# Kernel optimization log

Hardware: AMD Instinct MI355X
Metric: run time of the kernel (lower is better)

Reference implementation:

```python
import jax, jax.numpy as jnp
import numpy as np

T_STEPS = 16384  # sequence length T
N_DIM = 256      # input channels n
M_DIM = 512      # hidden/reservoir size m
K_MEM = 511      # memory rows K (addresses are 0..K, row 0 = 'no memory op')
L_OUT = 256      # output dims L


def setup_inputs() -> dict:
    key = jax.random.key(0)
    ks = jax.random.split(key, 10)
    s_ih = 1.0 / np.sqrt(N_DIM)
    s_hh = 1.0 / np.sqrt(M_DIM)
    X = jax.random.normal(ks[0], (T_STEPS, N_DIM), jnp.float32)
    h0 = jnp.zeros((M_DIM,), jnp.float32)  # init_state = zeros(m)
    # torch.nn.GRU parameters (single layer): weight_ih [3m, n], weight_hh [3m, m]
    W_ih = jax.random.normal(ks[1], (3 * M_DIM, N_DIM), jnp.float32) * s_ih
    W_hh = jax.random.normal(ks[2], (3 * M_DIM, M_DIM), jnp.float32) * s_hh
    b_ih = jax.random.normal(ks[3], (3 * M_DIM,), jnp.float32) * s_hh
    b_hh = jax.random.normal(ks[4], (3 * M_DIM,), jnp.float32) * s_hh
    # C_: Linear(m, K+1) -> memory address logits
    C_w = jax.random.normal(ks[5], (K_MEM + 1, M_DIM), jnp.float32) * s_hh
    C_b = jax.random.normal(ks[6], (K_MEM + 1,), jnp.float32) * s_hh
    # V_: Linear(m, L) -> outputs
    V_w = jax.random.normal(ks[7], (L_OUT, M_DIM), jnp.float32) * s_hh
    V_b = jax.random.normal(ks[8], (L_OUT,), jnp.float32) * s_hh
    return {"X": X, "h0": h0, "W_ih": W_ih, "W_hh": W_hh, "b_ih": b_ih,
            "b_hh": b_hh, "C_w": C_w, "C_b": C_b, "V_w": V_w, "V_b": V_b}


def reference(X, h0, W_ih, W_hh, b_ih, b_hh, C_w, C_b, V_w, V_b):
    m = h0.shape[0]
    n_addr = C_b.shape[0]  # K + 1

    def step(carry, x):
        h, M, written = carry
        # GRU cell (torch semantics)
        gi = W_ih @ x + b_ih          # [3m]
        gh = W_hh @ h + b_hh          # [3m]
        i_r, i_z, i_n = jnp.split(gi, 3)
        h_r, h_z, h_n = jnp.split(gh, 3)
        r = jax.nn.sigmoid(i_r + h_r)
        z = jax.nn.sigmoid(i_z + h_z)
        ng = jnp.tanh(i_n + r * h_n)
        h_new = (1.0 - z) * ng + z * h
        # discrete memory addressing via argmax over C_(h)
        logits = C_w @ h_new + C_b    # [K+1]
        q = jnp.argmax(logits)
        mem_q = M[q]                  # gather (read before write)
        has_entry = written[q] & (q > 0)
        # if address already written: read memory, replacing h
        h_out = jnp.where(has_entry, mem_q, h_new)
        # if address new (and > 0): write h into memory
        do_write = (q > 0) & jnp.logical_not(written[q])
        write_val = jnp.where(do_write, h_new, mem_q)  # no-op write otherwise
        M = M.at[q].set(write_val)
        written = written.at[q].set(written[q] | (q > 0))
        return (h_out, M, written), h_out

    M0 = jnp.zeros((n_addr, m), X.dtype)       # q_0 = 0 -> memory starts empty
    written0 = jnp.zeros((n_addr,), jnp.bool_)
    _, H = jax.lax.scan(step, (h0, M0, written0), X)  # H: [T, m]
    Y = H @ V_w.T + V_b                          # [T, L]
    return Y
```

## Files before the change

kernel.cpp:

```cpp
#include <hip/hip_runtime.h>
#include <stdint.h>

#define T_STEPS 16384
#define NDIM 256
#define MDIM 512
#define KP1 512
#define LOUT 256
#define G 16
#define TPB 256

typedef unsigned long long u64;
typedef unsigned int u32;

constexpr size_t OFF_GH    = 0;
constexpr size_t OFF_GHS   = 512ull * 1536;
constexpr size_t OFF_M     = OFF_GHS + 1536;
constexpr size_t OFF_RING  = OFF_M + 512ull * 512;
constexpr size_t OFF_H     = OFF_RING + 4ull * 1536;
constexpr size_t OFF_VWT   = OFF_H + 16384ull * 512;
constexpr size_t OFF_FLAGS = OFF_VWT + 512ull * 256;

__device__ __forceinline__ float ld_cohf(const float* p) {
  return __hip_atomic_load(p, __ATOMIC_RELAXED, __HIP_MEMORY_SCOPE_AGENT);
}
__device__ __forceinline__ void st_cohf(float* p, float v) {
  __hip_atomic_store(p, v, __ATOMIC_RELAXED, __HIP_MEMORY_SCOPE_AGENT);
}
__device__ __forceinline__ u64 ld_flag(const u64* p) {
  return __hip_atomic_load(p, __ATOMIC_RELAXED, __HIP_MEMORY_SCOPE_AGENT);
}
__device__ __forceinline__ void st_flag_rel(u64* p, u64 v) {
  __hip_atomic_store(p, v, __ATOMIC_RELEASE, __HIP_MEMORY_SCOPE_AGENT);
}
__device__ __forceinline__ void st_flag_rlx(u64* p, u64 v) {
  __hip_atomic_store(p, v, __ATOMIC_RELAXED, __HIP_MEMORY_SCOPE_AGENT);
}

__device__ __forceinline__ float sigm(float x) {
  return __builtin_amdgcn_rcpf(1.0f + __expf(-x));
}
__device__ __forceinline__ float tanh_(float x) {
  return 1.0f - 2.0f * __builtin_amdgcn_rcpf(__expf(2.0f * x) + 1.0f);
}

template<int CTRL>
__device__ __forceinline__ u32 dppmax(u32 v) {
  u32 t = (u32)__builtin_amdgcn_update_dpp(0, (int)v, CTRL, 0xf, 0xf, true);
  return v > t ? v : t;
}
__device__ __forceinline__ u32 wave_max_u32(u32 v) {
  v = dppmax<0x111>(v);
  v = dppmax<0x112>(v);
  v = dppmax<0x114>(v);
  v = dppmax<0x118>(v);
  v = dppmax<0x142>(v);
  v = dppmax<0x143>(v);
  return (u32)__builtin_amdgcn_readlane((int)v, 63);
}
__device__ __forceinline__ u32 row16_max_u32(u32 v) {
  v = dppmax<0x111>(v);
  v = dppmax<0x112>(v);
  v = dppmax<0x114>(v);
  v = dppmax<0x118>(v);
  return (u32)__builtin_amdgcn_readlane((int)v, 15);
}

__global__ __launch_bounds__(TPB, 1) void dmm_main(
    const float* __restrict__ X, const float* __restrict__ h0,
    const float* __restrict__ W_ih, const float* __restrict__ W_hh,
    const float* __restrict__ b_ih, const float* __restrict__ b_hh,
    const float* __restrict__ C_w, const float* __restrict__ C_b,
    float* __restrict__ ws)
{
  const int b   = blockIdx.x;
  const int tid = threadIdx.x;
  const int w   = tid >> 6;
  const int l   = tid & 63;

  float* GH   = ws + OFF_GH;
  float* GHS  = ws + OFF_GHS;
  float* Mrow = ws + OFF_M;
  float* RING = ws + OFF_RING;
  float* H    = ws + OFF_H;
  u64*   F    = (u64*)(ws + OFF_FLAGS);

  __shared__ __align__(16) float hnew[MDIM];
  __shared__ __align__(16) float red[96 * 36];
  __shared__ u32 written[KP1];
  __shared__ u32 bcw;

  const int pw   = (w >= 1) ? (w - 1) : 0;
  const int rloc = pw * 32 + (l >> 4) * 8;
  float wih[8][16];
  {
    int rbase = 96 * b + rloc;
    int cbase = 16 * (l & 15);
#pragma unroll
    for (int i = 0; i < 8; i++)
#pragma unroll
      for (int k = 0; k < 16; k++)
        wih[i][k] = W_ih[(size_t)(rbase + i) * NDIM + cbase + k];
  }
  float bihr[8];
#pragma unroll
  for (int i = 0; i < 8; i++) bihr[i] = b_ih[96 * b + rloc + i];

  float cw[4][16];
  {
    int rbase = 32 * b + w * 8 + (l >> 5) * 4;
    int cbase = 16 * (l & 31);
#pragma unroll
    for (int i = 0; i < 4; i++)
#pragma unroll
      for (int k = 0; k < 16; k++)
        cw[i][k] = C_w[(size_t)(rbase + i) * MDIM + cbase + k];
  }

  for (int i = tid; i < KP1; i += TPB) written[i] = 0u;
  if (tid == 0) bcw = 0u;
  hnew[tid]       = h0[tid];
  hnew[tid + 256] = h0[tid + 256];
  __syncthreads();

  float xreg[16];
  auto prefetchX = [&](int s) {
    int cbase = 16 * (l & 15);
#pragma unroll
    for (int k = 0; k < 16; k++) xreg[k] = X[(size_t)s * NDIM + cbase + k];
  };

  auto produce_gi = [&](int s) {
    float p[8];
#pragma unroll
    for (int i = 0; i < 8; i++) {
      float a = 0.f;
#pragma unroll
      for (int k = 0; k < 16; k++) a = fmaf(wih[i][k], xreg[k], a);
      p[i] = a;
    }
#pragma unroll
    for (int off = 1; off <= 8; off <<= 1) {
#pragma unroll
      for (int i = 0; i < 8; i++) p[i] += __shfl_xor(p[i], off, 64);
    }
    if ((l & 15) == 0) {
      float* dst = &RING[(size_t)(s & 3) * 1536 + 96 * b + rloc];
#pragma unroll
      for (int i = 0; i < 8; i++) st_cohf(&dst[i], p[i] + bihr[i]);
    }
  };

  auto compute_gh = [&](float* dst) {
    int cb = 16 * (l & 31);
    float hr[16];
#pragma unroll
    for (int k = 0; k < 16; k += 4) *(float4*)&hr[k] = *(const float4*)&hnew[cb + k];
    int rb = 96 * b + w * 24 + (l >> 5) * 12;
    float p[12];
#pragma unroll
    for (int i = 0; i < 12; i++) {
      float a = 0.f;
      const float* wr = &W_hh[(size_t)(rb + i) * MDIM + cb];
#pragma unroll
      for (int k = 0; k < 16; k++) a = fmaf(wr[k], hr[k], a);
      p[i] = a;
    }
    int rl = w * 24 + (l >> 5) * 12;
    int lc = l & 31;
#pragma unroll
    for (int i = 0; i < 12; i++) red[(rl + i) * 36 + lc] = p[i];
    __syncthreads();
    if (tid < 96) {
      float a = 0.f;
#pragma unroll
      for (int k = 0; k < 32; k += 4) {
        float4 v = *(const float4*)&red[tid * 36 + k];
        a += v.x + v.y + v.z + v.w;
      }
      a += b_hh[96 * b + tid];
      st_cohf(&dst[96 * b + tid], a);
    }
    __syncthreads();
  };

  if (w >= 1) {
    prefetchX(0); produce_gi(0);
    prefetchX(1); produce_gi(1);
    prefetchX(2); produce_gi(2);
    prefetchX(3);
  }
  __syncthreads();
  compute_gh(GHS);
  if (tid == 0) st_flag_rel(&F[b], 1ull);
  if (w == 0) {
    int guard = 0;
    bool done = false;
    while (!done) {
      u64 v = (l < G) ? ld_flag(&F[l]) : 1ull;
      done = (__ballot((int)(v == 1ull)) == ~0ull);
      if (++guard > (1 << 22)) break;
    }
  }
  __syncthreads();

  const float* ghsrc = GHS;
  bool prevReadHit = false;
  int  qprev = 0;

  for (int t = 0; t < T_STEPS; ++t) {
    float g0 = ld_cohf(&ghsrc[tid]);
    float g1 = ld_cohf(&ghsrc[tid + 256]);
    float g2 = ld_cohf(&ghsrc[512 + tid]);
    float g3 = ld_cohf(&ghsrc[512 + tid + 256]);
    float g4 = ld_cohf(&ghsrc[1024 + tid]);
    float g5 = ld_cohf(&ghsrc[1024 + tid + 256]);
    float m0 = 0.f, m1 = 0.f;
    if (prevReadHit) {
      m0 = ld_cohf(&Mrow[(size_t)qprev * 512 + tid]);
      m1 = ld_cohf(&Mrow[(size_t)qprev * 512 + tid + 256]);
    }
    const float* gi = &RING[(size_t)(t & 3) * 1536];
    float i0 = ld_cohf(&gi[tid]);
    float i1 = ld_cohf(&gi[tid + 256]);
    float i2 = ld_cohf(&gi[512 + tid]);
    float i3 = ld_cohf(&gi[512 + tid + 256]);
    float i4 = ld_cohf(&gi[1024 + tid]);
    float i5 = ld_cohf(&gi[1024 + tid + 256]);

    if (prevReadHit) {
      H[(size_t)(t - 1) * 512 + tid]       = m0;
      H[(size_t)(t - 1) * 512 + tid + 256] = m1;
    }

    float hp0 = prevReadHit ? m0 : hnew[tid];
    float hp1 = prevReadHit ? m1 : hnew[tid + 256];
    float r0 = sigm(i0 + g0), r1 = sigm(i1 + g1);
    float z0 = sigm(i2 + g2), z1 = sigm(i3 + g3);
    float n0 = tanh_(fmaf(r0, g4, i4)), n1 = tanh_(fmaf(r1, g5, i5));
    float hn0 = fmaf(z0, hp0 - n0, n0);
    float hn1 = fmaf(z1, hp1 - n1, n1);
    hnew[tid]       = hn0;
    hnew[tid + 256] = hn1;
    __syncthreads();

    {
      int cb = 16 * (l & 31);
      float hr[16];
#pragma unroll
      for (int k = 0; k < 16; k += 4) *(float4*)&hr[k] = *(const float4*)&hnew[cb + k];
      float p0 = 0.f, p1 = 0.f, p2 = 0.f, p3 = 0.f;
#pragma unroll
      for (int k = 0; k < 16; k++) {
        p0 = fmaf(cw[0][k], hr[k], p0);
        p1 = fmaf(cw[1][k], hr[k], p1);
        p2 = fmaf(cw[2][k], hr[k], p2);
        p3 = fmaf(cw[3][k], hr[k], p3);
      }
      int rl = w * 8 + (l >> 5) * 4;
      int lc = l & 31;
      red[(rl + 0) * 36 + lc] = p0;
      red[(rl + 1) * 36 + lc] = p1;
      red[(rl + 2) * 36 + lc] = p2;
      red[(rl + 3) * 36 + lc] = p3;
    }
    __syncthreads();

    u64 ownkey = 0;
    if (w <= 1) {
      u32 ord = 0;
      if (l < 32) {
        const float4* rp = (const float4*)&red[l * 36];
        float4 v0 = rp[0], v1 = rp[1], v2 = rp[2], v3 = rp[3];
        float4 v4 = rp[4], v5 = rp[5], v6 = rp[6], v7 = rp[7];
        double d0 = ((double)v0.x + (double)v0.y) + ((double)v0.z + (double)v0.w);
        double d1 = ((double)v1.x + (double)v1.y) + ((double)v1.z + (double)v1.w);
        double d2 = ((double)v2.x + (double)v2.y) + ((double)v2.z + (double)v2.w);
        double d3 = ((double)v3.x + (double)v3.y) + ((double)v3.z + (double)v3.w);
        double d4 = ((double)v4.x + (double)v4.y) + ((double)v4.z + (double)v4.w);
        double d5 = ((double)v5.x + (double)v5.y) + ((double)v5.z + (double)v5.w);
        double d6 = ((double)v6.x + (double)v6.y) + ((double)v6.z + (double)v6.w);
        double d7 = ((double)v7.x + (double)v7.y) + ((double)v7.z + (double)v7.w);
        double a = (((d0 + d1) + (d2 + d3)) + ((d4 + d5) + (d6 + d7)))
                 + (double)C_b[32 * b + l];
        float af = (float)a;
        u32 bits = __float_as_uint(af);
        ord = (bits & 0x80000000u) ? ~bits : (bits | 0x80000000u);
      }
      u32 maxord = wave_max_u32(ord);
      u64 mask = __ballot((int)(ord == maxord));
      int lane = __builtin_ctzll(mask);
      u64 key41 = ((u64)maxord << 9) | (u64)(511 - (32 * b + lane));
      if (tid == 64)
        st_flag_rlx(&F[16 + (size_t)(t & 1) * 16 + b], ((u64)(t + 1) << 41) | key41);
      ownkey = key41;
    }

    if (w >= 1 && t + 3 < T_STEPS) {
      produce_gi(t + 3);
      if (t + 4 < T_STEPS) prefetchX(t + 4);
    }

    u32 info;
    if (w == 0) {
      const bool need = (l < G) && (l != b);
      const u64* fp = &F[16 + (size_t)(t & 1) * 16 + l];
      u64 vp = need ? ld_flag(fp) : 0;
      int guard = 0;
      u64 v;
      for (;;) {
        u64 vn = need ? ld_flag(fp) : 0;
        bool ok = !need || ((vp >> 41) == (u64)(t + 1));
        if (__ballot((int)ok) == ~0ull) { v = vp; break; }
        vp = vn;
        if (++guard > (1 << 22)) { v = vp; break; }
      }
      u64 key = (l < G) ? ((l == b) ? ownkey : (v & ((1ull << 41) - 1))) : 0;
      u32 o = (u32)(key >> 9);
      u32 maxo = row16_max_u32(o);
      u32 cand = (o == maxo && l < G) ? (u32)(key & 511u) : 0u;
      u32 best = row16_max_u32(cand);
      int q = 511 - (int)best;
      u32 vinfo = 0;
      if (l == 0) {
        u32 wr = written[q];
        u32 fresh = (q > 0 && wr == 0u) ? 1u : 0u;
        u32 rhit  = (q > 0 && wr != 0u) ? 1u : 0u;
        if (fresh) written[q] = 1u;
        vinfo = (u32)q | (fresh << 16) | (rhit << 17);
      }
      vinfo = (u32)__builtin_amdgcn_readfirstlane((int)vinfo);
      info = vinfo;
      if (l == 0)
        __hip_atomic_store(&bcw, (vinfo << 4) | ((u32)(t + 1) & 0xFu),
                           __ATOMIC_RELEASE, __HIP_MEMORY_SCOPE_WORKGROUP);
    } else {
      u32 v;
      int guard = 0;
      for (;;) {
        v = __hip_atomic_load(&bcw, __ATOMIC_ACQUIRE, __HIP_MEMORY_SCOPE_WORKGROUP);
        if ((v & 0xFu) == ((u32)(t + 1) & 0xFu)) break;
        if (++guard > (1 << 25)) break;
      }
      info = v >> 4;
    }
    int  q     = (int)(info & 0xFFFFu);
    bool fresh = (info >> 16) & 1u;
    bool rhit  = (info >> 17) & 1u;

    if (!rhit) {
      H[(size_t)t * 512 + tid]       = hnew[tid];
      H[(size_t)t * 512 + tid + 256] = hnew[tid + 256];
      float* dst;
      if (fresh) {
        if (tid < 32) st_cohf(&Mrow[(size_t)q * 512 + 32 * b + tid], hnew[32 * b + tid]);
        dst = &GH[(size_t)q * 1536];
      } else {
        dst = GHS;
      }
      compute_gh(dst);
      if (tid == 0) st_flag_rel(&F[48 + (size_t)(t & 1) * 16 + b], (u64)(t + 1));
      if (w == 0) {
        int guard = 0;
        for (;;) {
          u64 v = (l < G) ? ld_flag(&F[48 + (size_t)(t & 1) * 16 + l]) : 0;
          bool ok = (l >= G) || (v == (u64)(t + 1));
          if (__ballot((int)ok) == ~0ull) break;
          if (++guard > (1 << 22)) break;
        }
      }
      __syncthreads();
      ghsrc = dst;
      prevReadHit = false;
    } else {
      ghsrc = &GH[(size_t)q * 1536];
      prevReadHit = true;
      qprev = q;
    }
  }

  if (prevReadHit) {
    float a = ld_cohf(&Mrow[(size_t)qprev * 512 + tid]);
    float c = ld_cohf(&Mrow[(size_t)qprev * 512 + tid + 256]);
    H[(size_t)(T_STEPS - 1) * 512 + tid]       = a;
    H[(size_t)(T_STEPS - 1) * 512 + tid + 256] = c;
  }
}

__global__ void vw_transpose(const float* __restrict__ Vw, float* __restrict__ VwT) {
  int idx = blockIdx.x * 256 + threadIdx.x;
  int kk = idx >> 8, ll = idx & 255;
  VwT[idx] = Vw[(size_t)ll * MDIM + kk];
}

__global__ __launch_bounds__(256) void y_gemm(const float* __restrict__ Hm,
                                              const float* __restrict__ VwT,
                                              const float* __restrict__ Vb,
                                              float* __restrict__ Y) {
  int t0 = blockIdx.x * 16;
  int tid = threadIdx.x;
  __shared__ __align__(16) float hs[16 * MDIM];
  for (int i = tid; i < 16 * MDIM; i += 256)
    hs[i] = Hm[(size_t)t0 * MDIM + i];
  __syncthreads();
  float acc[16];
  float vb = Vb[tid];
#pragma unroll
  for (int r = 0; r < 16; r++) acc[r] = vb;
  for (int k = 0; k < MDIM; k += 4) {
    float v0 = VwT[(size_t)(k + 0) * LOUT + tid];
    float v1 = VwT[(size_t)(k + 1) * LOUT + tid];
    float v2 = VwT[(size_t)(k + 2) * LOUT + tid];
    float v3 = VwT[(size_t)(k + 3) * LOUT + tid];
#pragma unroll
    for (int r = 0; r < 16; r++) {
      float4 h4 = *(const float4*)&hs[r * MDIM + k];
      acc[r] = fmaf(h4.x, v0, fmaf(h4.y, v1, fmaf(h4.z, v2, fmaf(h4.w, v3, acc[r]))));
    }
  }
#pragma unroll
  for (int r = 0; r < 16; r++)
    Y[(size_t)(t0 + r) * LOUT + tid] = acc[r];
}

extern "C" void kernel_launch(void* const* d_in, const int* in_sizes, int n_in,
                              void* d_out, int out_size, void* d_ws, size_t ws_size,
                              hipStream_t stream) {
  const float* X    = (const float*)d_in[0];
  const float* h0   = (const float*)d_in[1];
  const float* W_ih = (const float*)d_in[2];
  const float* W_hh = (const float*)d_in[3];
  const float* b_ih = (const float*)d_in[4];
  const float* b_hh = (const float*)d_in[5];
  const float* C_w  = (const float*)d_in[6];
  const float* C_b  = (const float*)d_in[7];
  const float* V_w  = (const float*)d_in[8];
  const float* V_b  = (const float*)d_in[9];
  float* ws  = (float*)d_ws;
  float* VwT = ws + OFF_VWT;
  float* Hm  = ws + OFF_H;

  hipLaunchKernelGGL(vw_transpose, dim3(512), dim3(256), 0, stream, V_w, VwT);
  hipLaunchKernelGGL(dmm_main, dim3(G), dim3(TPB), 0, stream,
                     X, h0, W_ih, W_hh, b_ih, b_hh, C_w, C_b, ws);
  hipLaunchKernelGGL(y_gemm, dim3(T_STEPS / 16), dim3(256), 0, stream,
                     Hm, VwT, V_b, (float*)d_out);
}
```

Before: 43.96 ms.

## Pad inter-block flags to separate lines and compute argmax redundantly per wave

Each 64-bit flag in the global flag array now sits 8 words apart, so the flags no longer share cache lines and polling blocks should contend less. The wave-0 leader that computed the address and handed it to the other waves through a shared-memory mailbox is removed. Every wave now does the row reduction, polls the peer flags and computes the argmax itself, then reads the written table directly. A __syncthreads is added before the written-table update to prevent a race. The cost is more flag polling traffic from all waves and redundant reduction work.

```diff
diff --git a/kernel.cpp b/kernel.cpp
--- a/kernel.cpp
+++ b/kernel.cpp
@@ -87,7 +87,6 @@
   __shared__ __align__(16) float hnew[MDIM];
   __shared__ __align__(16) float red[96 * 36];
   __shared__ u32 written[KP1];
-  __shared__ u32 bcw;
 
   const int pw   = (w >= 1) ? (w - 1) : 0;
   const int rloc = pw * 32 + (l >> 4) * 8;
@@ -117,7 +116,6 @@
   }
 
   for (int i = tid; i < KP1; i += TPB) written[i] = 0u;
-  if (tid == 0) bcw = 0u;
   hnew[tid]       = h0[tid];
   hnew[tid + 256] = h0[tid + 256];
   __syncthreads();
@@ -191,12 +189,12 @@
   }
   __syncthreads();
   compute_gh(GHS);
-  if (tid == 0) st_flag_rel(&F[b], 1ull);
+  if (tid == 0) st_flag_rel(&F[(size_t)b * 8], 1ull);
   if (w == 0) {
     int guard = 0;
     bool done = false;
     while (!done) {
-      u64 v = (l < G) ? ld_flag(&F[l]) : 1ull;
+      u64 v = (l < G) ? ld_flag(&F[(size_t)l * 8]) : 1ull;
       done = (__ballot((int)(v == 1ull)) == ~0ull);
       if (++guard > (1 << 22)) break;
     }
@@ -265,8 +263,8 @@
     }
     __syncthreads();
 
-    u64 ownkey = 0;
-    if (w <= 1) {
+    u64 ownkey;
+    {
       u32 ord = 0;
       if (l < 32) {
         const float4* rp = (const float4*)&red[l * 36];
@@ -289,10 +287,10 @@
       u32 maxord = wave_max_u32(ord);
       u64 mask = __ballot((int)(ord == maxord));
       int lane = __builtin_ctzll(mask);
-      u64 key41 = ((u64)maxord << 9) | (u64)(511 - (32 * b + lane));
+      ownkey = ((u64)maxord << 9) | (u64)(511 - (32 * b + lane));
       if (tid == 64)
-        st_flag_rlx(&F[16 + (size_t)(t & 1) * 16 + b], ((u64)(t + 1) << 41) | key41);
-      ownkey = key41;
+        st_flag_rlx(&F[(16 + (size_t)(t & 1) * 16 + b) * 8],
+                    ((u64)(t + 1) << 41) | ownkey);
     }
 
     if (w >= 1 && t + 3 < T_STEPS) {
@@ -300,10 +298,10 @@
       if (t + 4 < T_STEPS) prefetchX(t + 4);
     }
 
-    u32 info;
-    if (w == 0) {
+    int q;
+    {
       const bool need = (l < G) && (l != b);
-      const u64* fp = &F[16 + (size_t)(t & 1) * 16 + l];
+      const u64* fp = &F[(16 + (size_t)(t & 1) * 16 + l) * 8];
       u64 vp = need ? ld_flag(fp) : 0;
       int guard = 0;
       u64 v;
@@ -319,37 +317,17 @@
       u32 maxo = row16_max_u32(o);
       u32 cand = (o == maxo && l < G) ? (u32)(key & 511u) : 0u;
       u32 best = row16_max_u32(cand);
-      int q = 511 - (int)best;
-      u32 vinfo = 0;
-      if (l == 0) {
-        u32 wr = written[q];
-        u32 fresh = (q > 0 && wr == 0u) ? 1u : 0u;
-        u32 rhit  = (q > 0 && wr != 0u) ? 1u : 0u;
-        if (fresh) written[q] = 1u;
-        vinfo = (u32)q | (fresh << 16) | (rhit << 17);
-      }
-      vinfo = (u32)__builtin_amdgcn_readfirstlane((int)vinfo);
-      info = vinfo;
-      if (l == 0)
-        __hip_atomic_store(&bcw, (vinfo << 4) | ((u32)(t + 1) & 0xFu),
-                           __ATOMIC_RELEASE, __HIP_MEMORY_SCOPE_WORKGROUP);
-    } else {
-      u32 v;
-      int guard = 0;
-      for (;;) {
-        v = __hip_atomic_load(&bcw, __ATOMIC_ACQUIRE, __HIP_MEMORY_SCOPE_WORKGROUP);
-        if ((v & 0xFu) == ((u32)(t + 1) & 0xFu)) break;
-        if (++guard > (1 << 25)) break;
-      }
-      info = v >> 4;
-    }
-    int  q     = (int)(info & 0xFFFFu);
-    bool fresh = (info >> 16) & 1u;
-    bool rhit  = (info >> 17) & 1u;
+      q = 511 - (int)best;
+    }
+    u32 wr = written[q];
+    bool fresh = (q > 0 && wr == 0u);
+    bool rhit  = (q > 0 && wr != 0u);
 
     if (!rhit) {
       H[(size_t)t * 512 + tid]       = hnew[tid];
       H[(size_t)t * 512 + tid + 256] = hnew[tid + 256];
+      __syncthreads();
+      if (tid == 0 && fresh) written[q] = 1u;
       float* dst;
       if (fresh) {
         if (tid < 32) st_cohf(&Mrow[(size_t)q * 512 + 32 * b + tid], hnew[32 * b + tid]);
@@ -358,11 +336,11 @@
         dst = GHS;
       }
       compute_gh(dst);
-      if (tid == 0) st_flag_rel(&F[48 + (size_t)(t & 1) * 16 + b], (u64)(t + 1));
+      if (tid == 0) st_flag_rel(&F[(48 + (size_t)(t & 1) * 16 + b) * 8], (u64)(t + 1));
       if (w == 0) {
         int guard = 0;
         for (;;) {
-          u64 v = (l < G) ? ld_flag(&F[48 + (size_t)(t & 1) * 16 + l]) : 0;
+          u64 v = (l < G) ? ld_flag(&F[(48 + (size_t)(t & 1) * 16 + l) * 8]) : 0;
           bool ok = (l >= G) || (v == (u64)(t + 1));
           if (__ballot((int)ok) == ~0ull) break;
           if (++guard > (1 << 22)) break;
```

Result: slower. 50.50 ms (+14.9%).
